# Performance work log

Hardware: AMD Instinct MI355X
Metric: run time of the kernel (lower is better)

The kernel has to match this reference:

```python
import jax, jax.numpy as jnp
import numpy as np

DIM = 768
HEADS = 12
HEAD_DIM = DIM // HEADS
SCALE = HEAD_DIM ** -0.5
EPS = 1e-6


def setup_inputs() -> dict:
    key = jax.random.key(0)
    ks = jax.random.split(key, 10)
    B, Nq, Nk, C = 4, 4096, 4096, DIM
    std = C ** -0.5
    return {
        "x_q": jax.random.normal(ks[0], (B, Nq, C), jnp.float32),
        "x_kv": jax.random.normal(ks[1], (B, Nk, C), jnp.float32),
        "Wq": jax.random.normal(ks[2], (C, C), jnp.float32) * std,
        "bq": jnp.zeros((C,), jnp.float32),
        "Wk": jax.random.normal(ks[3], (C, C), jnp.float32) * std,
        "bk": jnp.zeros((C,), jnp.float32),
        "Wv": jax.random.normal(ks[4], (C, C), jnp.float32) * std,
        "bv": jnp.zeros((C,), jnp.float32),
        "Wp": jax.random.normal(ks[5], (C, C), jnp.float32) * std,
        "bp": jnp.zeros((C,), jnp.float32),
    }


def _phi(x):
    # ELU(alpha=1) + 1 positive feature map
    return jax.nn.elu(x) + 1.0


def reference(x_q, x_kv, Wq, bq, Wk, bk, Wv, bv, Wp, bp):
    B, Nq, C = x_q.shape
    Nk = x_kv.shape[1]
    h, d = HEADS, HEAD_DIM
    # projections (torch Linear: x @ W.T + b)
    q = x_q @ Wq.T + bq   # [B,Nq,C]
    k = x_kv @ Wk.T + bk  # [B,Nk,C]
    v = x_kv @ Wv.T + bv  # [B,Nk,C]
    # split heads -> [B,h,N,d]
    q = q.reshape(B, Nq, h, d).transpose(0, 2, 1, 3) * SCALE
    k = k.reshape(B, Nk, h, d).transpose(0, 2, 1, 3)
    v = v.reshape(B, Nk, h, d).transpose(0, 2, 1, 3)
    q_phi = _phi(q)
    k_phi = _phi(k)
    # KV state [B,h,d,d] and normalizer sum [B,h,d]
    kv = jnp.einsum('bhnd,bhne->bhde', k_phi, v)
    k_sum = k_phi.sum(axis=2)
    out = jnp.einsum('bhnd,bhde->bhne', q_phi, kv)
    z = jnp.einsum('bhnd,bhd->bhn', q_phi, k_sum)[..., None] + EPS
    out = out / z
    out = out.transpose(0, 2, 1, 3).reshape(B, Nq, C)
    return out @ Wp.T + bp
```

## Files before the change

### kernel.cpp

```cpp
#include <hip/hip_runtime.h>
#include <hip/hip_bf16.h>
#include <cstdint>
#include <cstddef>

#define HD_B   4
#define SEQ    4096
#define CDIM   768
#define HEADS  12
#define HDIM   64
#define MROWS  (HD_B * SEQ)
#define QSCALE 0.125f
#define EPSV   1e-6f

typedef __attribute__((ext_vector_type(8))) short  short8v;
typedef __attribute__((ext_vector_type(4))) float  f32x4;

__device__ __forceinline__ unsigned short f2b(float f) {
    unsigned int u = __float_as_uint(f);
    u += 0x7FFFu + ((u >> 16) & 1u);
    return (unsigned short)(u >> 16);
}
__device__ __forceinline__ float b2f(unsigned short b) {
    return __uint_as_float(((unsigned int)b) << 16);
}
__device__ __forceinline__ float phi_f(float x) {
    return x > 0.f ? x + 1.f : __expf(x);
}

#define GLOAD_LDS16(g, l)                                             \
    __builtin_amdgcn_global_load_lds(                                 \
        (__attribute__((address_space(1))) void*)(void*)(g),          \
        (__attribute__((address_space(3))) void*)(l), 16, 0, 0)

__global__ void wcvt_all(const float* __restrict__ wk, const float* __restrict__ wv,
                         const float* __restrict__ wq, const float* __restrict__ wp,
                         unsigned short* __restrict__ dst) {
    const int y = blockIdx.y;
    const float* src = (y == 0) ? wk : (y == 1) ? wv : (y == 2) ? wq : wp;
    const int i = blockIdx.x * 256 + threadIdx.x;
    float4 v = reinterpret_cast<const float4*>(src)[i];
    ushort4 o;
    o.x = f2b(v.x); o.y = f2b(v.y); o.z = f2b(v.z); o.w = f2b(v.w);
    reinterpret_cast<ushort4*>(dst + (size_t)y * (CDIM * CDIM))[i] = o;
}

template <int EPI, int AFP32>
__global__ __launch_bounds__(256) void gemm_bt(
    const void* __restrict__ Ain,
    const unsigned short* __restrict__ Bw,
    const float* __restrict__ bias0,
    const float* __restrict__ bias1,
    void* __restrict__ out0,
    void* __restrict__ out1)
{
    constexpr int K = CDIM;
    __shared__ __align__(16) char smem[32768];
    auto As = (unsigned short (*)[64])(smem);
    auto Bs = (unsigned short (*)[64])(smem + 16384);

    const int tid  = threadIdx.x;
    const int lane = tid & 63;
    const int w    = tid >> 6;
    const int wr   = w >> 1;
    const int wc   = w & 1;
    const int brow = blockIdx.x * 128;
    const int bcol = blockIdx.y * 128;

    f32x4 acc[4][4];
#pragma unroll
    for (int i = 0; i < 4; ++i)
#pragma unroll
        for (int j = 0; j < 4; ++j)
            acc[i][j] = (f32x4){0.f, 0.f, 0.f, 0.f};

    const int r8 = lane >> 3;
    const int c8 = ((lane & 7) ^ r8) << 3;
    const int ar = lane >> 4;
    const int ac = (lane & 15) << 2;
    const int fr  = lane & 15;
    const int hi4 = lane >> 4;

    const float* A32          = (const float*)Ain;
    const unsigned short* A16 = (const unsigned short*)Ain;

    for (int k0 = 0; k0 < K; k0 += 64) {
#pragma unroll
        for (int g = 0; g < 4; ++g) {
            const unsigned short* src =
                Bw + (size_t)(bcol + w * 32 + g * 8 + r8) * K + k0 + c8;
            GLOAD_LDS16(src, (char*)Bs + (w * 32 + g * 8) * 128);
        }
        if (AFP32) {
#pragma unroll
            for (int j = 0; j < 8; ++j) {
                const int row = w * 32 + j * 4 + ar;
                float4 f = *(const float4*)(A32 + (size_t)(brow + row) * K + k0 + ac);
                unsigned int p0, p1;
                asm("v_cvt_pk_bf16_f32 %0, %1, %2" : "=v"(p0) : "v"(f.x), "v"(f.y));
                asm("v_cvt_pk_bf16_f32 %0, %1, %2" : "=v"(p1) : "v"(f.z), "v"(f.w));
                const int off = row * 128 + (((ac << 1)) ^ ((row & 7) << 4));
                uint2 pk; pk.x = p0; pk.y = p1;
                *(uint2*)((char*)As + off) = pk;
            }
        } else {
#pragma unroll
            for (int g = 0; g < 4; ++g) {
                const unsigned short* src =
                    A16 + (size_t)(brow + w * 32 + g * 8 + r8) * K + k0 + c8;
                GLOAD_LDS16(src, (char*)As + (w * 32 + g * 8) * 128);
            }
        }
        __syncthreads();

        short8v a[4][2], b[4][2];
#pragma unroll
        for (int i = 0; i < 4; ++i) {
            const int row = wr * 64 + i * 16 + fr;
#pragma unroll
            for (int ks = 0; ks < 2; ++ks) {
                const int off = row * 128 + ((((ks << 2) + hi4) ^ (row & 7)) << 4);
                a[i][ks] = *(const short8v*)((const char*)As + off);
            }
        }
#pragma unroll
        for (int j = 0; j < 4; ++j) {
            const int row = wc * 64 + j * 16 + fr;
#pragma unroll
            for (int ks = 0; ks < 2; ++ks) {
                const int off = row * 128 + ((((ks << 2) + hi4) ^ (row & 7)) << 4);
                b[j][ks] = *(const short8v*)((const char*)Bs + off);
            }
        }
#pragma unroll
        for (int i = 0; i < 4; ++i)
#pragma unroll
            for (int j = 0; j < 4; ++j) {
                acc[i][j] = __builtin_amdgcn_mfma_f32_16x16x32_bf16(
                    a[i][0], b[j][0], acc[i][j], 0, 0, 0);
                acc[i][j] = __builtin_amdgcn_mfma_f32_16x16x32_bf16(
                    a[i][1], b[j][1], acc[i][j], 0, 0, 0);
            }
        __syncthreads();
    }

    float* ep = (float*)smem + w * (16 * 68);
    const int rr = lane >> 2;
    const int cb = (lane & 3) * 4;

    const bool isV = (EPI == 1) && (bcol >= 768);
    const float* bptr = (EPI == 1 && isV) ? (bias1 + (bcol - 768)) : (bias0 + bcol);
    const int colbase = (isV ? bcol - 768 : bcol) + wc * 64;
    unsigned short* o16 = (unsigned short*)(isV ? out1 : out0);
    float* o32 = (float*)out0;

    float4 bb[4];
#pragma unroll
    for (int q = 0; q < 4; ++q)
        bb[q] = *(const float4*)&bptr[wc * 64 + q * 16 + cb];

#pragma unroll
    for (int i = 0; i < 4; ++i) {
#pragma unroll
        for (int j = 0; j < 4; ++j)
#pragma unroll
            for (int r = 0; r < 4; ++r)
                ep[(hi4 * 4 + r) * 68 + j * 16 + fr] = acc[i][j][r];
#pragma unroll
        for (int q = 0; q < 4; ++q) {
            const int cc = q * 16 + cb;
            f32x4 v = *(const f32x4*)&ep[rr * 68 + cc];
            const int rg = brow + wr * 64 + i * 16 + rr;
            const int cg = colbase + cc;
            const float4 bq = bb[q];
            if (EPI == 0) {
                ushort4 ov;
                ov.x = f2b(phi_f((v[0] + bq.x) * QSCALE));
                ov.y = f2b(phi_f((v[1] + bq.y) * QSCALE));
                ov.z = f2b(phi_f((v[2] + bq.z) * QSCALE));
                ov.w = f2b(phi_f((v[3] + bq.w) * QSCALE));
                *(ushort4*)(o16 + (size_t)rg * 768 + cg) = ov;
            } else if (EPI == 1) {
                ushort4 ov;
                if (!isV) {
                    ov.x = f2b(phi_f(v[0] + bq.x));
                    ov.y = f2b(phi_f(v[1] + bq.y));
                    ov.z = f2b(phi_f(v[2] + bq.z));
                    ov.w = f2b(phi_f(v[3] + bq.w));
                } else {
                    ov.x = f2b(v[0] + bq.x);
                    ov.y = f2b(v[1] + bq.y);
                    ov.z = f2b(v[2] + bq.z);
                    ov.w = f2b(v[3] + bq.w);
                }
                *(ushort4*)(o16 + (size_t)rg * 768 + cg) = ov;
            } else {
                float4 ov;
                ov.x = v[0] + bq.x; ov.y = v[1] + bq.y;
                ov.z = v[2] + bq.z; ov.w = v[3] + bq.w;
                *(float4*)(o32 + (size_t)rg * 768 + cg) = ov;
            }
        }
    }
}

#define KVCH   128
#define KVITER 2
#define NCHUNK 16

__global__ __launch_bounds__(256) void kv_part(
    const unsigned short* __restrict__ kphi,
    const unsigned short* __restrict__ vmat,
    float* __restrict__ part)
{
    const int bh = blockIdx.y;
    const int b  = bh / HEADS, h = bh % HEADS;
    const int c  = blockIdx.x;
    __shared__ float Kl[KVCH][HDIM];
    __shared__ float Vl[KVCH][HDIM];
    const int t  = threadIdx.x;
    const int i  = t >> 2;
    const int jb = t & 3;

    float acc[16];
#pragma unroll
    for (int jj = 0; jj < 16; ++jj) acc[jj] = 0.f;
    float ksum = 0.f;

    for (int it = 0; it < KVITER; ++it) {
        const size_t rbase = (size_t)b * SEQ + (size_t)c * (KVCH * KVITER) + it * KVCH;
        __syncthreads();
        for (int l = 0; l < KVCH / 32; ++l) {
            int row = l * 32 + (t >> 3);
            int col = (t & 7) << 3;
            const size_t g = (rbase + row) * CDIM + h * HDIM + col;
            int4 kk = *(const int4*)(kphi + g);
            int4 vv = *(const int4*)(vmat + g);
            const unsigned short* kp = (const unsigned short*)&kk;
            const unsigned short* vp = (const unsigned short*)&vv;
#pragma unroll
            for (int q = 0; q < 8; ++q) {
                Kl[row][col + q] = b2f(kp[q]);
                Vl[row][col + q] = b2f(vp[q]);
            }
        }
        __syncthreads();
        for (int n = 0; n < KVCH; ++n) {
            float kf = Kl[n][i];
            const float4* vr = (const float4*)&Vl[n][jb * 16];
            float4 v0 = vr[0], v1 = vr[1], v2 = vr[2], v3 = vr[3];
            acc[0]  += kf * v0.x; acc[1]  += kf * v0.y; acc[2]  += kf * v0.z; acc[3]  += kf * v0.w;
            acc[4]  += kf * v1.x; acc[5]  += kf * v1.y; acc[6]  += kf * v1.z; acc[7]  += kf * v1.w;
            acc[8]  += kf * v2.x; acc[9]  += kf * v2.y; acc[10] += kf * v2.z; acc[11] += kf * v2.w;
            acc[12] += kf * v3.x; acc[13] += kf * v3.y; acc[14] += kf * v3.z; acc[15] += kf * v3.w;
            ksum += kf;
        }
    }
    float* op = part + ((size_t)c * 48 + bh) * 4160;
#pragma unroll
    for (int jj = 0; jj < 16; ++jj) op[i * 64 + jb * 16 + jj] = acc[jj];
    if (jb == 0) op[4096 + i] = ksum;
}

__global__ void kv_finalize(const float* __restrict__ part, float* __restrict__ kv) {
    int idx = blockIdx.x * 256 + threadIdx.x;
    if (idx >= 48 * 4160) return;
    float s = 0.f;
    for (int c = 0; c < NCHUNK; ++c) s += part[(size_t)c * 48 * 4160 + idx];
    kv[idx] = s;
}

__global__ __launch_bounds__(256) void attn_apply(
    const unsigned short* __restrict__ qphi,
    const float* __restrict__ kv,
    unsigned short* __restrict__ attn)
{
    const int h  = blockIdx.y;
    const int m0 = blockIdx.x * 64;
    const int b  = m0 >> 12;
    const int bh = b * HEADS + h;
    __shared__ float kvs[HDIM][HDIM];
    __shared__ float ksums[HDIM];
    __shared__ unsigned short ql[64][HDIM];
    const int t = threadIdx.x;
    const float* kvp = kv + (size_t)bh * 4160;
#pragma unroll
    for (int it = 0; it < 4; ++it) {
        int e = it * 1024 + t * 4;
        *(float4*)&kvs[e >> 6][e & 63] = *(const float4*)&kvp[e];
    }
    if (t < 64) ksums[t] = kvp[4096 + t];
#pragma unroll
    for (int it = 0; it < 2; ++it) {
        int row = it * 32 + (t >> 3);
        int col = (t & 7) << 3;
        *(int4*)&ql[row][col] =
            *(const int4*)(qphi + (size_t)(m0 + row) * CDIM + h * HDIM + col);
    }
    __syncthreads();

    const int r  = t >> 2;
    const int jb = t & 3;
    float acc[16];
#pragma unroll
    for (int jj = 0; jj < 16; ++jj) acc[jj] = 0.f;
    float z = 0.f;
    for (int q8 = 0; q8 < 8; ++q8) {
        short8v qv = *(const short8v*)&ql[r][q8 * 8];
#pragma unroll
        for (int dd = 0; dd < 8; ++dd) {
            float qd = b2f((unsigned short)qv[dd]);
            int d = q8 * 8 + dd;
            const float4* kr = (const float4*)&kvs[d][jb * 16];
            float4 k0 = kr[0], k1 = kr[1], k2 = kr[2], k3 = kr[3];
            acc[0]  += qd * k0.x; acc[1]  += qd * k0.y; acc[2]  += qd * k0.z; acc[3]  += qd * k0.w;
            acc[4]  += qd * k1.x; acc[5]  += qd * k1.y; acc[6]  += qd * k1.z; acc[7]  += qd * k1.w;
            acc[8]  += qd * k2.x; acc[9]  += qd * k2.y; acc[10] += qd * k2.z; acc[11] += qd * k2.w;
            acc[12] += qd * k3.x; acc[13] += qd * k3.y; acc[14] += qd * k3.z; acc[15] += qd * k3.w;
            z += qd * ksums[d];
        }
    }
    const float inv = 1.f / (z + EPSV);
    unsigned short* op = attn + (size_t)(m0 + r) * CDIM + h * HDIM + jb * 16;
#pragma unroll
    for (int jj = 0; jj < 16; ++jj) op[jj] = f2b(acc[jj] * inv);
}

extern "C" void kernel_launch(void* const* d_in, const int* in_sizes, int n_in,
                              void* d_out, int out_size, void* d_ws, size_t ws_size,
                              hipStream_t stream)
{
    const float* x_q  = (const float*)d_in[0];
    const float* x_kv = (const float*)d_in[1];
    const float* Wq   = (const float*)d_in[2];
    const float* bq   = (const float*)d_in[3];
    const float* Wk   = (const float*)d_in[4];
    const float* bk   = (const float*)d_in[5];
    const float* Wv   = (const float*)d_in[6];
    const float* bv   = (const float*)d_in[7];
    const float* Wp   = (const float*)d_in[8];
    const float* bp   = (const float*)d_in[9];
    float* out = (float*)d_out;

    char* ws = (char*)d_ws;
    size_t off = 0;
    auto alloc = [&](size_t bytes) -> char* {
        char* p = ws + off;
        off += (bytes + 255) & ~(size_t)255;
        return p;
    };
    const size_t xbytes = (size_t)MROWS * CDIM * 2;
    const size_t wbytes = (size_t)CDIM * CDIM * 2;
    unsigned short* w16   = (unsigned short*)alloc(4 * wbytes);
    unsigned short* wk16  = w16;
    unsigned short* wq16  = w16 + 2 * (CDIM * CDIM);
    unsigned short* wp16  = w16 + 3 * (CDIM * CDIM);
    unsigned short* qphi  = (unsigned short*)alloc(xbytes);
    unsigned short* kphi  = (unsigned short*)alloc(xbytes);
    unsigned short* v16   = (unsigned short*)alloc(xbytes);
    unsigned short* attn16 = (unsigned short*)alloc(xbytes);
    float* part = (float*)alloc((size_t)NCHUNK * 48 * 4160 * 4);
    float* kvf  = (float*)alloc((size_t)48 * 4160 * 4);

    wcvt_all<<<dim3(576, 4), 256, 0, stream>>>(Wk, Wv, Wq, Wp, w16);

    gemm_bt<0, 1><<<dim3(128, 6), 256, 0, stream>>>(
        (const void*)x_q, wq16, bq, nullptr, (void*)qphi, nullptr);
    gemm_bt<1, 1><<<dim3(128, 12), 256, 0, stream>>>(
        (const void*)x_kv, wk16, bk, bv, (void*)kphi, (void*)v16);

    kv_part<<<dim3(NCHUNK, 48), 256, 0, stream>>>(kphi, v16, part);
    kv_finalize<<<(48 * 4160 + 255) / 256, 256, 0, stream>>>(part, kvf);
    attn_apply<<<dim3(MROWS / 64, HEADS), 256, 0, stream>>>(qphi, kvf, attn16);

    gemm_bt<2, 0><<<dim3(128, 6), 256, 0, stream>>>(
        (const void*)attn16, wp16, bp, nullptr, (void*)out, nullptr);
}
```

Baseline: 232.1 us.

## Double-buffer GEMM K-loop, merge Q/K/V projections, swizzle block order

```diff
diff --git a/kernel.cpp b/kernel.cpp
--- a/kernel.cpp
+++ b/kernel.cpp
@@ -32,11 +32,11 @@
         (__attribute__((address_space(1))) void*)(void*)(g),          \
         (__attribute__((address_space(3))) void*)(l), 16, 0, 0)
 
-__global__ void wcvt_all(const float* __restrict__ wk, const float* __restrict__ wv,
-                         const float* __restrict__ wq, const float* __restrict__ wp,
+__global__ void wcvt_all(const float* __restrict__ wq, const float* __restrict__ wk,
+                         const float* __restrict__ wv, const float* __restrict__ wp,
                          unsigned short* __restrict__ dst) {
     const int y = blockIdx.y;
-    const float* src = (y == 0) ? wk : (y == 1) ? wv : (y == 2) ? wq : wp;
+    const float* src = (y == 0) ? wq : (y == 1) ? wk : (y == 2) ? wv : wp;
     const int i = blockIdx.x * 256 + threadIdx.x;
     float4 v = reinterpret_cast<const float4*>(src)[i];
     ushort4 o;
@@ -44,27 +44,49 @@
     reinterpret_cast<ushort4*>(dst + (size_t)y * (CDIM * CDIM))[i] = o;
 }
 
-template <int EPI, int AFP32>
-__global__ __launch_bounds__(256) void gemm_bt(
-    const void* __restrict__ Ain,
-    const unsigned short* __restrict__ Bw,
-    const float* __restrict__ bias0,
-    const float* __restrict__ bias1,
-    void* __restrict__ out0,
-    void* __restrict__ out1)
+template <int KIND>
+__global__ __launch_bounds__(256) void gemm_pipe(
+    const float* __restrict__ Aq,
+    const float* __restrict__ Akv,
+    const unsigned short* __restrict__ Abf,
+    const unsigned short* __restrict__ Wb,
+    const float* __restrict__ b0,
+    const float* __restrict__ b1,
+    const float* __restrict__ b2,
+    unsigned short* __restrict__ out_q,
+    unsigned short* __restrict__ out_k,
+    unsigned short* __restrict__ out_v,
+    float* __restrict__ out_f)
 {
-    constexpr int K = CDIM;
-    __shared__ __align__(16) char smem[32768];
-    auto As = (unsigned short (*)[64])(smem);
-    auto Bs = (unsigned short (*)[64])(smem + 16384);
+    constexpr int K  = CDIM;
+    constexpr int NC = (KIND == 0) ? 18 : 6;
+    constexpr int T  = NC * 128;
+    constexpr int NT = K / 64;
+
+    __shared__ __align__(16) char smem[65536];
 
     const int tid  = threadIdx.x;
     const int lane = tid & 63;
     const int w    = tid >> 6;
-    const int wr   = w >> 1;
-    const int wc   = w & 1;
-    const int brow = blockIdx.x * 128;
-    const int bcol = blockIdx.y * 128;
+    const int wr   = w >> 1, wc = w & 1;
+
+    const int bid  = blockIdx.x;
+    const int s    = (bid & 7) * (T >> 3) + (bid >> 3);
+    const int colp = s % NC;
+    const int rowp = s / NC;
+    const int brow = rowp * 128;
+    const int mode = (KIND == 0) ? (colp / 6) : 3;
+    const int bcol = (KIND == 0) ? (colp % 6) * 128 : colp * 128;
+
+    const float* A32 = (KIND == 0) ? (mode == 0 ? Aq : Akv) : nullptr;
+    const unsigned short* Bp = Wb + ((KIND == 0) ? (size_t)mode * (K * K) : 0);
+
+    const int r8  = lane >> 3;
+    const int c8  = ((lane & 7) ^ r8) << 3;
+    const int ar  = lane >> 4;
+    const int ac  = (lane & 15) << 2;
+    const int fr  = lane & 15;
+    const int hi4 = lane >> 4;
 
     f32x4 acc[4][4];
 #pragma unroll
@@ -73,90 +95,111 @@
         for (int j = 0; j < 4; ++j)
             acc[i][j] = (f32x4){0.f, 0.f, 0.f, 0.f};
 
-    const int r8 = lane >> 3;
-    const int c8 = ((lane & 7) ^ r8) << 3;
-    const int ar = lane >> 4;
-    const int ac = (lane & 15) << 2;
-    const int fr  = lane & 15;
-    const int hi4 = lane >> 4;
-
-    const float* A32          = (const float*)Ain;
-    const unsigned short* A16 = (const unsigned short*)Ain;
-
-    for (int k0 = 0; k0 < K; k0 += 64) {
+    auto stageB = [&](int buf, int k0) {
+        char* dst = smem + 32768 + buf * 16384;
 #pragma unroll
         for (int g = 0; g < 4; ++g) {
             const unsigned short* src =
-                Bw + (size_t)(bcol + w * 32 + g * 8 + r8) * K + k0 + c8;
-            GLOAD_LDS16(src, (char*)Bs + (w * 32 + g * 8) * 128);
-        }
-        if (AFP32) {
-#pragma unroll
-            for (int j = 0; j < 8; ++j) {
-                const int row = w * 32 + j * 4 + ar;
-                float4 f = *(const float4*)(A32 + (size_t)(brow + row) * K + k0 + ac);
-                unsigned int p0, p1;
-                asm("v_cvt_pk_bf16_f32 %0, %1, %2" : "=v"(p0) : "v"(f.x), "v"(f.y));
-                asm("v_cvt_pk_bf16_f32 %0, %1, %2" : "=v"(p1) : "v"(f.z), "v"(f.w));
-                const int off = row * 128 + (((ac << 1)) ^ ((row & 7) << 4));
-                uint2 pk; pk.x = p0; pk.y = p1;
-                *(uint2*)((char*)As + off) = pk;
-            }
-        } else {
-#pragma unroll
-            for (int g = 0; g < 4; ++g) {
-                const unsigned short* src =
-                    A16 + (size_t)(brow + w * 32 + g * 8 + r8) * K + k0 + c8;
-                GLOAD_LDS16(src, (char*)As + (w * 32 + g * 8) * 128);
-            }
-        }
-        __syncthreads();
-
-        short8v a[4][2], b[4][2];
+                Bp + (size_t)(bcol + w * 32 + g * 8 + r8) * K + k0 + c8;
+            GLOAD_LDS16(src, dst + (w * 32 + g * 8) * 128);
+        }
+    };
+    auto stageA16 = [&](int buf, int k0) {
+        char* dst = smem + buf * 16384;
+#pragma unroll
+        for (int g = 0; g < 4; ++g) {
+            const unsigned short* src =
+                Abf + (size_t)(brow + w * 32 + g * 8 + r8) * K + k0 + c8;
+            GLOAD_LDS16(src, dst + (w * 32 + g * 8) * 128);
+        }
+    };
+    auto loadA32 = [&](int k0, float4* f) {
+#pragma unroll
+        for (int j = 0; j < 8; ++j) {
+            const int row = w * 32 + j * 4 + ar;
+            f[j] = *(const float4*)(A32 + (size_t)(brow + row) * K + k0 + ac);
+        }
+    };
+    auto writeA32 = [&](int buf, const float4* f) {
+        char* dst = smem + buf * 16384;
+#pragma unroll
+        for (int j = 0; j < 8; ++j) {
+            const int row = w * 32 + j * 4 + ar;
+            unsigned int p0, p1;
+            asm("v_cvt_pk_bf16_f32 %0, %1, %2" : "=v"(p0) : "v"(f[j].x), "v"(f[j].y));
+            asm("v_cvt_pk_bf16_f32 %0, %1, %2" : "=v"(p1) : "v"(f[j].z), "v"(f[j].w));
+            uint2 pk; pk.x = p0; pk.y = p1;
+            *(uint2*)(dst + row * 128 + ((ac << 1) ^ ((row & 7) << 4))) = pk;
+        }
+    };
+    auto compute = [&](int buf) {
+        const char* Ab = smem + buf * 16384;
+        const char* Bb = smem + 32768 + buf * 16384;
+        short8v a[4][2];
 #pragma unroll
         for (int i = 0; i < 4; ++i) {
             const int row = wr * 64 + i * 16 + fr;
 #pragma unroll
-            for (int ks = 0; ks < 2; ++ks) {
-                const int off = row * 128 + ((((ks << 2) + hi4) ^ (row & 7)) << 4);
-                a[i][ks] = *(const short8v*)((const char*)As + off);
-            }
+            for (int ks = 0; ks < 2; ++ks)
+                a[i][ks] = *(const short8v*)(Ab + row * 128 +
+                              ((((ks << 2) + hi4) ^ (row & 7)) << 4));
         }
 #pragma unroll
         for (int j = 0; j < 4; ++j) {
             const int row = wc * 64 + j * 16 + fr;
-#pragma unroll
-            for (int ks = 0; ks < 2; ++ks) {
-                const int off = row * 128 + ((((ks << 2) + hi4) ^ (row & 7)) << 4);
-                b[j][ks] = *(const short8v*)((const char*)Bs + off);
+            short8v bb0 = *(const short8v*)(Bb + row * 128 + ((hi4 ^ (row & 7)) << 4));
+            short8v bb1 = *(const short8v*)(Bb + row * 128 + (((4 + hi4) ^ (row & 7)) << 4));
+#pragma unroll
+            for (int i = 0; i < 4; ++i) {
+                acc[i][j] = __builtin_amdgcn_mfma_f32_16x16x32_bf16(a[i][0], bb0, acc[i][j], 0, 0, 0);
+                acc[i][j] = __builtin_amdgcn_mfma_f32_16x16x32_bf16(a[i][1], bb1, acc[i][j], 0, 0, 0);
             }
         }
-#pragma unroll
-        for (int i = 0; i < 4; ++i)
-#pragma unroll
-            for (int j = 0; j < 4; ++j) {
-                acc[i][j] = __builtin_amdgcn_mfma_f32_16x16x32_bf16(
-                    a[i][0], b[j][0], acc[i][j], 0, 0, 0);
-                acc[i][j] = __builtin_amdgcn_mfma_f32_16x16x32_bf16(
-                    a[i][1], b[j][1], acc[i][j], 0, 0, 0);
+    };
+
+    if (KIND == 0) {
+        float4 fA[8];
+        stageB(0, 0);
+        loadA32(0, fA);
+        asm volatile("s_waitcnt vmcnt(0)" ::: "memory");
+        writeA32(0, fA);
+        __syncthreads();
+        for (int t = 0; t < NT; ++t) {
+            const int cur = t & 1, nxt = cur ^ 1;
+            if (t < NT - 1) { stageB(nxt, (t + 1) * 64); loadA32((t + 1) * 64, fA); }
+            __builtin_amdgcn_sched_barrier(0);
+            compute(cur);
+            if (t < NT - 1) {
+                asm volatile("s_waitcnt vmcnt(0)" ::: "memory");
+                writeA32(nxt, fA);
+                __syncthreads();
             }
+        }
+    } else {
+        stageB(0, 0);
+        stageA16(0, 0);
         __syncthreads();
-    }
-
-    float* ep = (float*)smem + w * (16 * 68);
+        for (int t = 0; t < NT; ++t) {
+            const int cur = t & 1, nxt = cur ^ 1;
+            if (t < NT - 1) { stageB(nxt, (t + 1) * 64); stageA16(nxt, (t + 1) * 64); }
+            __builtin_amdgcn_sched_barrier(0);
+            compute(cur);
+            if (t < NT - 1) __syncthreads();
+        }
+    }
+    __syncthreads();
+
+    float* ep = (float*)(void*)smem + w * (16 * 68);
     const int rr = lane >> 2;
     const int cb = (lane & 3) * 4;
-
-    const bool isV = (EPI == 1) && (bcol >= 768);
-    const float* bptr = (EPI == 1 && isV) ? (bias1 + (bcol - 768)) : (bias0 + bcol);
-    const int colbase = (isV ? bcol - 768 : bcol) + wc * 64;
-    unsigned short* o16 = (unsigned short*)(isV ? out1 : out0);
-    float* o32 = (float*)out0;
+    const float* bptr = (KIND == 1) ? b0 : (mode == 0 ? b0 : (mode == 1 ? b1 : b2));
+    unsigned short* o16 = (KIND == 0)
+        ? (mode == 0 ? out_q : (mode == 1 ? out_k : out_v)) : nullptr;
 
     float4 bb[4];
 #pragma unroll
     for (int q = 0; q < 4; ++q)
-        bb[q] = *(const float4*)&bptr[wc * 64 + q * 16 + cb];
+        bb[q] = *(const float4*)&bptr[bcol + wc * 64 + q * 16 + cb];
 
 #pragma unroll
     for (int i = 0; i < 4; ++i) {
@@ -170,18 +213,21 @@
             const int cc = q * 16 + cb;
             f32x4 v = *(const f32x4*)&ep[rr * 68 + cc];
             const int rg = brow + wr * 64 + i * 16 + rr;
-            const int cg = colbase + cc;
+            const int cg = bcol + wc * 64 + cc;
             const float4 bq = bb[q];
-            if (EPI == 0) {
+            if (KIND == 1) {
+                float4 ov;
+                ov.x = v[0] + bq.x; ov.y = v[1] + bq.y;
+                ov.z = v[2] + bq.z; ov.w = v[3] + bq.w;
+                *(float4*)(out_f + (size_t)rg * 768 + cg) = ov;
+            } else {
                 ushort4 ov;
-                ov.x = f2b(phi_f((v[0] + bq.x) * QSCALE));
-                ov.y = f2b(phi_f((v[1] + bq.y) * QSCALE));
-                ov.z = f2b(phi_f((v[2] + bq.z) * QSCALE));
-                ov.w = f2b(phi_f((v[3] + bq.w) * QSCALE));
-                *(ushort4*)(o16 + (size_t)rg * 768 + cg) = ov;
-            } else if (EPI == 1) {
-                ushort4 ov;
-                if (!isV) {
+                if (mode == 0) {
+                    ov.x = f2b(phi_f((v[0] + bq.x) * QSCALE));
+                    ov.y = f2b(phi_f((v[1] + bq.y) * QSCALE));
+                    ov.z = f2b(phi_f((v[2] + bq.z) * QSCALE));
+                    ov.w = f2b(phi_f((v[3] + bq.w) * QSCALE));
+                } else if (mode == 1) {
                     ov.x = f2b(phi_f(v[0] + bq.x));
                     ov.y = f2b(phi_f(v[1] + bq.y));
                     ov.z = f2b(phi_f(v[2] + bq.z));
@@ -193,11 +239,6 @@
                     ov.w = f2b(v[3] + bq.w);
                 }
                 *(ushort4*)(o16 + (size_t)rg * 768 + cg) = ov;
-            } else {
-                float4 ov;
-                ov.x = v[0] + bq.x; ov.y = v[1] + bq.y;
-                ov.z = v[2] + bq.z; ov.w = v[3] + bq.w;
-                *(float4*)(o32 + (size_t)rg * 768 + cg) = ov;
             }
         }
     }
@@ -350,28 +391,25 @@
     };
     const size_t xbytes = (size_t)MROWS * CDIM * 2;
     const size_t wbytes = (size_t)CDIM * CDIM * 2;
-    unsigned short* w16   = (unsigned short*)alloc(4 * wbytes);
-    unsigned short* wk16  = w16;
-    unsigned short* wq16  = w16 + 2 * (CDIM * CDIM);
-    unsigned short* wp16  = w16 + 3 * (CDIM * CDIM);
-    unsigned short* qphi  = (unsigned short*)alloc(xbytes);
-    unsigned short* kphi  = (unsigned short*)alloc(xbytes);
-    unsigned short* v16   = (unsigned short*)alloc(xbytes);
+    unsigned short* w16    = (unsigned short*)alloc(4 * wbytes);
+    unsigned short* wp16   = w16 + 3 * (CDIM * CDIM);
+    unsigned short* qphi   = (unsigned short*)alloc(xbytes);
+    unsigned short* kphi   = (unsigned short*)alloc(xbytes);
+    unsigned short* v16    = (unsigned short*)alloc(xbytes);
     unsigned short* attn16 = (unsigned short*)alloc(xbytes);
     float* part = (float*)alloc((size_t)NCHUNK * 48 * 4160 * 4);
     float* kvf  = (float*)alloc((size_t)48 * 4160 * 4);
 
-    wcvt_all<<<dim3(576, 4), 256, 0, stream>>>(Wk, Wv, Wq, Wp, w16);
-
-    gemm_bt<0, 1><<<dim3(128, 6), 256, 0, stream>>>(
-        (const void*)x_q, wq16, bq, nullptr, (void*)qphi, nullptr);
-    gemm_bt<1, 1><<<dim3(128, 12), 256, 0, stream>>>(
-        (const void*)x_kv, wk16, bk, bv, (void*)kphi, (void*)v16);
+    wcvt_all<<<dim3(576, 4), 256, 0, stream>>>(Wq, Wk, Wv, Wp, w16);
+
+    gemm_pipe<0><<<2304, 256, 0, stream>>>(
+        x_q, x_kv, nullptr, w16, bq, bk, bv, qphi, kphi, v16, nullptr);
 
     kv_part<<<dim3(NCHUNK, 48), 256, 0, stream>>>(kphi, v16, part);
     kv_finalize<<<(48 * 4160 + 255) / 256, 256, 0, stream>>>(part, kvf);
     attn_apply<<<dim3(MROWS / 64, HEADS), 256, 0, stream>>>(qphi, kvf, attn16);
 
-    gemm_bt<2, 0><<<dim3(128, 6), 256, 0, stream>>>(
-        (const void*)attn16, wp16, bp, nullptr, (void*)out, nullptr);
-}
+    gemm_pipe<1><<<768, 256, 0, stream>>>(
+        nullptr, nullptr, attn16, wp16, bp, nullptr, nullptr,
+        nullptr, nullptr, nullptr, out);
+}
```

Measured after the change: 224.4 us. -3.3%, faster.
